# Performance work log

Hardware: AMD Instinct MI355X
Metric: run time of the kernel (lower is better)

The kernel has to match this reference:

```python
import jax, jax.numpy as jnp
import numpy as np

DIM, HEADS, RANK = 768, 12, 64
HEAD_DIM = DIM // HEADS

def _xavier(key, shape):
    fan_in, fan_out = shape[1], shape[0]
    std = (2.0 / (fan_in + fan_out)) ** 0.5
    return std * jax.random.normal(key, shape, dtype=jnp.float32)

def setup_inputs() -> dict:
    key = jax.random.key(0)
    ks = jax.random.split(key, 12)
    B, N = 8, 1024
    x = jax.random.normal(ks[0], (B, N, DIM), dtype=jnp.float32)
    params = {}
    for i, nm in enumerate(['Q', 'K', 'V']):
        params[f'W_{nm}0'] = _xavier(ks[1 + 3 * i], (DIM, RANK))
        params[f'W_{nm}1'] = _xavier(ks[2 + 3 * i], (HEADS, RANK))
        params[f'W_{nm}2'] = _xavier(ks[3 + 3 * i], (HEAD_DIM, RANK))
    proj_w = _xavier(ks[10], (DIM, DIM))
    proj_b = jnp.zeros((DIM,), dtype=jnp.float32)
    return dict(x=x, W_Q0=params['W_Q0'], W_Q1=params['W_Q1'], W_Q2=params['W_Q2'],
                W_K0=params['W_K0'], W_K1=params['W_K1'], W_K2=params['W_K2'],
                W_V0=params['W_V0'], W_V1=params['W_V1'], W_V2=params['W_V2'],
                proj_w=proj_w, proj_b=proj_b)

def _cp_proj(xh, W2, W1, W0, B, N, H, hd):
    # xh: [B,N,H,hd]; contract head_dim with W2 and heads with W1 -> [B,N,R], then expand to dim via W0
    t = jnp.einsum('blnd,dr,nr->blr', xh, W2, W1)
    out = jnp.einsum('blr,mr->blm', t, W0)          # [B,N,dim]
    return out.reshape(B, N, H, hd).transpose(0, 2, 1, 3)  # [B,H,N,hd]

def reference(x, W_Q0, W_Q1, W_Q2, W_K0, W_K1, W_K2, W_V0, W_V1, W_V2, proj_w, proj_b):
    B, N, C = x.shape
    H = W_Q1.shape[0]
    hd = C // H
    scale = hd ** -0.5
    xh = x.reshape(B, N, H, hd)
    q = _cp_proj(xh, W_Q2, W_Q1, W_Q0, B, N, H, hd)
    k = _cp_proj(xh, W_K2, W_K1, W_K0, B, N, H, hd)
    v = _cp_proj(xh, W_V2, W_V1, W_V0, B, N, H, hd)
    attn = jax.nn.softmax(jnp.einsum('bhqd,bhkd->bhqk', q, k) * scale, axis=-1)
    out = jnp.einsum('bhqk,bhkd->bhqd', attn, v).transpose(0, 2, 1, 3).reshape(B, N, C)
    return out @ proj_w.T + proj_b
```

## Files before the change

### kernel.cpp

```cpp
#include <hip/hip_runtime.h>

typedef unsigned short u16;
typedef __attribute__((ext_vector_type(8))) short bf16x8;
typedef __attribute__((ext_vector_type(4))) float f32x4;
typedef __attribute__((ext_vector_type(4))) unsigned short u16x4;
typedef __attribute__((ext_vector_type(8))) unsigned short u16x8;

#define AS1 __attribute__((address_space(1)))
#define AS3 __attribute__((address_space(3)))

__device__ __forceinline__ float b2f(u16 s) {
    return __uint_as_float(((unsigned)s) << 16);
}
__device__ __forceinline__ u16 f2b(float f) {
    unsigned u = __float_as_uint(f);
    unsigned r = 0x7fffu + ((u >> 16) & 1u);
    return (u16)((u + r) >> 16);
}

__device__ __forceinline__ unsigned packtrunc(float p0, float p1) {
#if __has_builtin(__builtin_amdgcn_perm)
    return __builtin_amdgcn_perm(__float_as_uint(p1), __float_as_uint(p0), 0x07060302u);
#else
    return (__float_as_uint(p0) >> 16) | (__float_as_uint(p1) & 0xffff0000u);
#endif
}

__device__ __forceinline__ void g2l16(const u16* g, u16* l) {
    __builtin_amdgcn_global_load_lds((const AS1 void*)g, (AS3 void*)l, 16, 0, 0);
}

#if __has_builtin(__builtin_amdgcn_exp2f)
#define EXP2(x) __builtin_amdgcn_exp2f(x)
#else
#define EXP2(x) exp2f(x)
#endif

__global__ __launch_bounds__(256) void build_prep(
    const float* __restrict__ Wq0, const float* __restrict__ Wq1, const float* __restrict__ Wq2,
    const float* __restrict__ Wk0, const float* __restrict__ Wk1, const float* __restrict__ Wk2,
    const float* __restrict__ Wv0, const float* __restrict__ Wv1, const float* __restrict__ Wv2,
    const float* __restrict__ PW,
    u16* __restrict__ G, u16* __restrict__ W0b, u16* __restrict__ Dcat)
{
    const int bx = blockIdx.x;
    const int t = threadIdx.x;
    if (bx < 1152) {
        const int idx = bx * 256 + t;
        if (idx < 147456) {
            const int row = idx / 768, c = idx - row * 768;
            const int which = row >> 6, r = row & 63;
            const int h = c >> 6, d = c & 63;
            const float* W1 = (which == 0) ? Wq1 : (which == 1) ? Wk1 : Wv1;
            const float* W2 = (which == 0) ? Wq2 : (which == 1) ? Wk2 : Wv2;
            G[idx] = f2b(W1[h * 64 + r] * W2[d * 64 + r]);
        } else {
            const int j = idx - 147456;
            const int row = j >> 6, r = j & 63;
            const int which = row / 768, mm = row - which * 768;
            const float* W0 = (which == 0) ? Wq0 : (which == 1) ? Wk0 : Wv0;
            const float scale = (which == 0) ? 0.125f * 1.4426950408889634f : 1.0f;
            W0b[j] = f2b(W0[mm * 64 + r] * scale);
        }
    } else {
        __shared__ float w0s[64 * 65];
        __shared__ float pws[32 * 65];
        const int hb = bx - 1152;
        const int h = hb / 24, mBase = (hb - h * 24) * 32;
        for (int i = t; i < 4096; i += 256) {
            const int d = i >> 6, r = i & 63;
            w0s[d * 65 + r] = Wv0[(h * 64 + d) * 64 + r];
        }
        for (int i = t; i < 2048; i += 256) {
            const int mi = i >> 6, d = i & 63;
            pws[mi * 65 + d] = PW[(size_t)(mBase + mi) * 768 + h * 64 + d];
        }
        __syncthreads();
        const int r = t & 63, mi0 = t >> 6;
        float w0c[64];
#pragma unroll
        for (int d = 0; d < 64; ++d) w0c[d] = w0s[d * 65 + r];
        for (int mi = mi0; mi < 32; mi += 4) {
            float acc = 0.f;
#pragma unroll
            for (int d = 0; d < 64; ++d) acc += pws[mi * 65 + d] * w0c[d];
            Dcat[(size_t)(mBase + mi) * 768 + h * 64 + r] = f2b(acc);
        }
    }
}

__global__ __launch_bounds__(256, 2) void gemm_t(
    const float* __restrict__ X, const u16* __restrict__ G,
    u16* __restrict__ T, u16* __restrict__ tvt)
{
    __shared__ u16 As[64 * 32];
    __shared__ u16 Bs[64 * 32];

    const int tid = threadIdx.x;
    const int lane = tid & 63, wv = tid >> 6;
    const int l15 = lane & 15, quad = lane >> 4;
    const int rowBase = blockIdx.y * 64;
    const int colBase = blockIdx.x * 64;

    const int srow = tid >> 2;
    const int scol = (tid & 3) * 8;
    const float* aS = X + (size_t)(rowBase + srow) * 768 + scol;
    const u16*  bS  = G + (size_t)(colBase + srow) * 768 + scol;

    float4 a0 = *(const float4*)(aS);
    float4 a1 = *(const float4*)(aS + 4);
    int4   b0 = *(const int4*)(bS);

    const f32x4 zero4 = {0.f, 0.f, 0.f, 0.f};
    f32x4 acc[4];
#pragma unroll
    for (int tn = 0; tn < 4; ++tn) acc[tn] = zero4;

    for (int kk = 0; kk < 768; kk += 32) {
        __syncthreads();
        u16x8 ap;
        ap[0] = f2b(a0.x); ap[1] = f2b(a0.y); ap[2] = f2b(a0.z); ap[3] = f2b(a0.w);
        ap[4] = f2b(a1.x); ap[5] = f2b(a1.y); ap[6] = f2b(a1.z); ap[7] = f2b(a1.w);
        *(u16x8*)&As[srow * 32 + scol] = ap;
        *(int4*)&Bs[srow * 32 + scol]  = b0;
        __syncthreads();

        if (kk < 736) {
            a0 = *(const float4*)(aS + kk + 32);
            a1 = *(const float4*)(aS + kk + 36);
            b0 = *(const int4*)(bS + kk + 32);
        }

        const bf16x8 af = *(const bf16x8*)(As + (wv * 16 + l15) * 32 + quad * 8);
#pragma unroll
        for (int tn = 0; tn < 4; ++tn) {
            const bf16x8 bf = *(const bf16x8*)(Bs + (tn * 16 + l15) * 32 + quad * 8);
            acc[tn] = __builtin_amdgcn_mfma_f32_16x16x32_bf16(af, bf, acc[tn], 0, 0, 0);
        }
    }

    if (colBase < 128) {
#pragma unroll
        for (int tn = 0; tn < 4; ++tn) {
            const int col = colBase + tn * 16 + l15;
#pragma unroll
            for (int r = 0; r < 4; ++r) {
                const int grow = rowBase + wv * 16 + quad * 4 + r;
                T[(size_t)grow * 128 + col] = f2b(acc[tn][r]);
            }
        }
    } else {
#pragma unroll
        for (int tn = 0; tn < 4; ++tn) {
            const int rr = tn * 16 + l15;
            const int grow = rowBase + wv * 16 + quad * 4;
            u16x4 pk;
            pk.x = f2b(acc[tn][0]); pk.y = f2b(acc[tn][1]);
            pk.z = f2b(acc[tn][2]); pk.w = f2b(acc[tn][3]);
            *(u16x4*)(tvt + (size_t)rr * 8192 + grow) = pk;
        }
    }
}

__global__ __launch_bounds__(256, 2) void gemm_expand(
    const u16* __restrict__ T, const u16* __restrict__ W0b, u16* __restrict__ qkp)
{
    __shared__ u16 As[128 * 32];
    __shared__ u16 Bs[128 * 32];

    const int tid  = threadIdx.x;
    const int lane = tid & 63, wv = tid >> 6;
    const int l15  = lane & 15, quad = lane >> 4;
    const int rowBase = blockIdx.y * 128;
    const int colBase = blockIdx.x * 128;
    const int which = blockIdx.x / 6;

    const int srow = wv * 32 + (lane >> 2);
    const int scol = (lane & 3) * 8;
    const u16* aSrc = T   + (size_t)(rowBase + srow) * 128 + which * 64 + scol;
    const u16* bSrc = W0b + (size_t)(colBase + srow) * 64 + scol;
    u16* aDst = As + wv * 1024;
    u16* bDst = Bs + wv * 1024;

    const f32x4 zero4 = {0.f, 0.f, 0.f, 0.f};
    f32x4 acc[4][4];
#pragma unroll
    for (int tm = 0; tm < 4; ++tm)
#pragma unroll
        for (int tn = 0; tn < 4; ++tn) acc[tm][tn] = zero4;

    const int wr = (wv >> 1) * 64, wc = (wv & 1) * 64;

    for (int kk = 0; kk < 64; kk += 32) {
        __syncthreads();
        g2l16(aSrc + kk,            aDst);
        g2l16(aSrc + kk + 16 * 128, aDst + 512);
        g2l16(bSrc + kk,            bDst);
        g2l16(bSrc + kk + 16 * 64,  bDst + 512);
        __syncthreads();

        bf16x8 af[4], bfm[4];
#pragma unroll
        for (int t = 0; t < 4; ++t) {
            af[t]  = *(const bf16x8*)(As + (wr + t * 16 + l15) * 32 + quad * 8);
            bfm[t] = *(const bf16x8*)(Bs + (wc + t * 16 + l15) * 32 + quad * 8);
        }
#pragma unroll
        for (int tm = 0; tm < 4; ++tm)
#pragma unroll
            for (int tn = 0; tn < 4; ++tn)
                acc[tm][tn] = __builtin_amdgcn_mfma_f32_16x16x32_bf16(
                    af[tm], bfm[tn], acc[tm][tn], 0, 0, 0);
    }

    const int mmBase = colBase - which * 768 + wc;
    u16* outp = qkp + (size_t)which * 6291456;
#pragma unroll
    for (int tm = 0; tm < 4; ++tm) {
        const int grow = rowBase + wr + tm * 16 + quad * 4;
        const int b = grow >> 10, l = grow & 1023;
#pragma unroll
        for (int tn = 0; tn < 4; ++tn) {
            const int mmv = mmBase + tn * 16 + l15;
            const int h = mmv >> 6, d = mmv & 63;
            const size_t base = (((size_t)(b * 12 + h) * 1024 + l) << 6) + d;
#pragma unroll
            for (int r = 0; r < 4; ++r)
                outp[base + (size_t)r * 64] = f2b(acc[tm][tn][r]);
        }
    }
}

__global__ __launch_bounds__(256, 3) void flash_attn6(
    const u16* __restrict__ qk, const u16* __restrict__ tvt, u16* __restrict__ Z)
{
    const int qt = blockIdx.x;
    const int bh = blockIdx.y;
    const int b = bh / 12, h = bh - b * 12;
    const u16* qp = qk + (size_t)bh * 65536 + qt * 8192;
    const u16* kp = qk + 6291456 + (size_t)bh * 65536;
    const u16* vp = tvt + b * 1024;

    __shared__ u16 Ks[64][72];
    __shared__ u16 Vs[64][72];

    const int t = threadIdx.x;
    const int lane = t & 63, wv = t >> 6;
    const int l15 = lane & 15, quad = lane >> 4;

    bf16x8 qf[2][2];
#pragma unroll
    for (int qg = 0; qg < 2; ++qg) {
        qf[qg][0] = *(const bf16x8*)(qp + (wv * 32 + qg * 16 + l15) * 64 + quad * 8);
        qf[qg][1] = *(const bf16x8*)(qp + (wv * 32 + qg * 16 + l15) * 64 + 32 + quad * 8);
    }

    const int srow = t >> 2;
    const int scol = (t & 3) * 16;
    const int p5 = srow & 31;
    const int lrow = (srow & 32) | ((p5 & 4) << 2) | ((p5 & 16) >> 1)
                   | ((p5 & 8) >> 1) | (p5 & 3);

    bf16x8 vone = {};
    if (l15 == 0) {
#pragma unroll
        for (int j = 0; j < 8; ++j) vone[j] = (short)0x3F80;
    }

    int4 kr0 = *(const int4*)(kp + srow * 64 + scol);
    int4 kr1 = *(const int4*)(kp + srow * 64 + scol + 8);
    int4 vr0 = *(const int4*)(vp + (size_t)srow * 8192 + scol);
    int4 vr1 = *(const int4*)(vp + (size_t)srow * 8192 + scol + 8);

    const f32x4 zero4 = {0.f, 0.f, 0.f, 0.f};
    f32x4 o_acc[2][4];
    f32x4 Lacc[2] = {zero4, zero4};
#pragma unroll
    for (int qg = 0; qg < 2; ++qg)
#pragma unroll
        for (int tn = 0; tn < 4; ++tn) o_acc[qg][tn] = zero4;

    for (int kt = 0; kt < 16; ++kt) {
        __syncthreads();
        *(int4*)&Ks[lrow][scol]     = kr0;
        *(int4*)&Ks[lrow][scol + 8] = kr1;
        *(int4*)&Vs[srow][scol]     = vr0;
        *(int4*)&Vs[srow][scol + 8] = vr1;
        __syncthreads();

        if (kt < 15) {
            kr0 = *(const int4*)(kp + (kt + 1) * 4096 + srow * 64 + scol);
            kr1 = *(const int4*)(kp + (kt + 1) * 4096 + srow * 64 + scol + 8);
            vr0 = *(const int4*)(vp + (size_t)srow * 8192 + (kt + 1) * 64 + scol);
            vr1 = *(const int4*)(vp + (size_t)srow * 8192 + (kt + 1) * 64 + scol + 8);
        }

        f32x4 Sacc[2][4];
#pragma unroll
        for (int qg = 0; qg < 2; ++qg)
#pragma unroll
            for (int tk = 0; tk < 4; ++tk) Sacc[qg][tk] = zero4;
#pragma unroll
        for (int ks = 0; ks < 2; ++ks) {
#pragma unroll
            for (int tk = 0; tk < 4; ++tk) {
                const bf16x8 kf = *(const bf16x8*)&Ks[tk * 16 + l15][ks * 32 + quad * 8];
                Sacc[0][tk] = __builtin_amdgcn_mfma_f32_16x16x32_bf16(kf, qf[0][ks], Sacc[0][tk], 0, 0, 0);
                Sacc[1][tk] = __builtin_amdgcn_mfma_f32_16x16x32_bf16(kf, qf[1][ks], Sacc[1][tk], 0, 0, 0);
            }
        }

        union { bf16x8 v; unsigned u[4]; } pf[2][2];
#pragma unroll
        for (int qg = 0; qg < 2; ++qg)
#pragma unroll
            for (int tk = 0; tk < 4; ++tk) {
                const float p0 = EXP2(Sacc[qg][tk][0]);
                const float p1 = EXP2(Sacc[qg][tk][1]);
                const float p2 = EXP2(Sacc[qg][tk][2]);
                const float p3 = EXP2(Sacc[qg][tk][3]);
                const int g = tk >> 1, hf = (tk & 1) * 2;
                pf[qg][g].u[hf + 0] = packtrunc(p0, p1);
                pf[qg][g].u[hf + 1] = packtrunc(p2, p3);
            }

#pragma unroll
        for (int g = 0; g < 2; ++g) {
#pragma unroll
            for (int tn = 0; tn < 4; ++tn) {
                const bf16x8 vf = *(const bf16x8*)&Vs[tn * 16 + l15][g * 32 + quad * 8];
                o_acc[0][tn] = __builtin_amdgcn_mfma_f32_16x16x32_bf16(pf[0][g].v, vf, o_acc[0][tn], 0, 0, 0);
                o_acc[1][tn] = __builtin_amdgcn_mfma_f32_16x16x32_bf16(pf[1][g].v, vf, o_acc[1][tn], 0, 0, 0);
            }
            Lacc[0] = __builtin_amdgcn_mfma_f32_16x16x32_bf16(pf[0][g].v, vone, Lacc[0], 0, 0, 0);
            Lacc[1] = __builtin_amdgcn_mfma_f32_16x16x32_bf16(pf[1][g].v, vone, Lacc[1], 0, 0, 0);
        }
    }

#pragma unroll
    for (int qg = 0; qg < 2; ++qg) {
#pragma unroll
        for (int r = 0; r < 4; ++r) {
            const float Lv = __shfl(Lacc[qg][r], quad << 4, 64);
            const float inv = 1.0f / Lv;
            const int token = qt * 128 + wv * 32 + qg * 16 + quad * 4 + r;
#pragma unroll
            for (int tn = 0; tn < 4; ++tn) {
                const int col = h * 64 + tn * 16 + l15;
                Z[(size_t)(b * 1024 + token) * 768 + col] = f2b(o_acc[qg][tn][r] * inv);
            }
        }
    }
}

__global__ __launch_bounds__(256, 3) void gemm_out(
    const u16* __restrict__ A, const u16* __restrict__ Bt,
    float* __restrict__ C, const float* __restrict__ bias)
{
    __shared__ u16 As[128 * 32];
    __shared__ u16 Bs[64 * 32];

    const int tid  = threadIdx.x;
    const int lane = tid & 63, wv = tid >> 6;
    const int l15  = lane & 15, quad = lane >> 4;
    const int rowBase = blockIdx.y * 128;
    const int colBase = blockIdx.x * 64;

    const int srowA = wv * 32 + (lane >> 2);
    const int srowB = wv * 16 + (lane >> 2);
    const int scol  = (lane & 3) * 8;
    const u16* aSrc = A  + (size_t)(rowBase + srowA) * 768 + scol;
    const u16* bSrc = Bt + (size_t)(colBase + srowB) * 768 + scol;
    u16* aDst = As + wv * 1024;
    u16* bDst = Bs + wv * 512;

    const f32x4 zero4 = {0.f, 0.f, 0.f, 0.f};
    f32x4 acc[2][4];
#pragma unroll
    for (int tm = 0; tm < 2; ++tm)
#pragma unroll
        for (int tn = 0; tn < 4; ++tn) acc[tm][tn] = zero4;

    for (int kk = 0; kk < 768; kk += 32) {
        __syncthreads();
        g2l16(aSrc + kk,            aDst);
        g2l16(aSrc + kk + 16 * 768, aDst + 512);
        g2l16(bSrc + kk,            bDst);
        __syncthreads();

        bf16x8 af[2], bfm[4];
#pragma unroll
        for (int t = 0; t < 2; ++t)
            af[t]  = *(const bf16x8*)(As + (wv * 32 + t * 16 + l15) * 32 + quad * 8);
#pragma unroll
        for (int t = 0; t < 4; ++t)
            bfm[t] = *(const bf16x8*)(Bs + (t * 16 + l15) * 32 + quad * 8);
#pragma unroll
        for (int tm = 0; tm < 2; ++tm)
#pragma unroll
            for (int tn = 0; tn < 4; ++tn)
                acc[tm][tn] = __builtin_amdgcn_mfma_f32_16x16x32_bf16(
                    af[tm], bfm[tn], acc[tm][tn], 0, 0, 0);
    }

#pragma unroll
    for (int tm = 0; tm < 2; ++tm) {
        const int grow = rowBase + wv * 32 + tm * 16 + quad * 4;
#pragma unroll
        for (int tn = 0; tn < 4; ++tn) {
            const int gcol = colBase + tn * 16 + l15;
            const float bv = bias[gcol];
#pragma unroll
            for (int r = 0; r < 4; ++r)
                C[(size_t)(grow + r) * 768 + gcol] = acc[tm][tn][r] + bv;
        }
    }
}

extern "C" void kernel_launch(void* const* d_in, const int* in_sizes, int n_in,
                              void* d_out, int out_size, void* d_ws, size_t ws_size,
                              hipStream_t stream)
{
    const float* x      = (const float*)d_in[0];
    const float* Wq0    = (const float*)d_in[1];
    const float* Wq1    = (const float*)d_in[2];
    const float* Wq2    = (const float*)d_in[3];
    const float* Wk0    = (const float*)d_in[4];
    const float* Wk1    = (const float*)d_in[5];
    const float* Wk2    = (const float*)d_in[6];
    const float* Wv0    = (const float*)d_in[7];
    const float* Wv1    = (const float*)d_in[8];
    const float* Wv2    = (const float*)d_in[9];
    const float* proj_w = (const float*)d_in[10];
    const float* proj_b = (const float*)d_in[11];
    float* outp = (float*)d_out;

    char* ws = (char*)d_ws;
    u16* T    = (u16*)ws;
    u16* tvt  = (u16*)(ws + 2097152);
    u16* G    = (u16*)(ws + 3145728);
    u16* W0b  = (u16*)(ws + 3440640);
    u16* Dcat = (u16*)(ws + 3735552);
    u16* Zcat = (u16*)(ws + 4915200);
    u16* qk   = (u16*)(ws + 17498112);

    build_prep<<<1440, 256, 0, stream>>>(Wq0, Wq1, Wq2, Wk0, Wk1, Wk2, Wv0, Wv1, Wv2,
                                         proj_w, G, W0b, Dcat);
    gemm_t<<<dim3(3, 128), 256, 0, stream>>>(x, G, T, tvt);
    gemm_expand<<<dim3(12, 64), 256, 0, stream>>>(T, W0b, qk);
    flash_attn6<<<dim3(8, 96), 256, 0, stream>>>(qk, tvt, Zcat);
    gemm_out<<<dim3(12, 64), 256, 0, stream>>>(Zcat, Dcat, outp, proj_b);
}
```

Before: 180.1 us.

## Fold Q expansion into per-head rank-space key matrix, skip Q materialization

Precomputes per-head M_h = Wq0_h^T Wk0_h (scaled) in rank space, so queries stay as the rank-64 T vectors and only K' = T_k M_h^T is expanded. This halves the expand GEMM grid and removes writing and reading the full Q tensor. Attention now reads Q rows straight from T with a 128-element stride. The grid order of the attention kernel is also swapped so blocks sharing a batch run together. Rounding changes because the combined weight is stored in bf16.

```diff
diff --git a/kernel.cpp b/kernel.cpp
--- a/kernel.cpp
+++ b/kernel.cpp
@@ -41,31 +41,40 @@
     const float* __restrict__ Wk0, const float* __restrict__ Wk1, const float* __restrict__ Wk2,
     const float* __restrict__ Wv0, const float* __restrict__ Wv1, const float* __restrict__ Wv2,
     const float* __restrict__ PW,
-    u16* __restrict__ G, u16* __restrict__ W0b, u16* __restrict__ Dcat)
+    u16* __restrict__ G, u16* __restrict__ Mqkb, u16* __restrict__ Dcat)
 {
     const int bx = blockIdx.x;
     const int t = threadIdx.x;
-    if (bx < 1152) {
+    if (bx < 576) {
         const int idx = bx * 256 + t;
-        if (idx < 147456) {
-            const int row = idx / 768, c = idx - row * 768;
-            const int which = row >> 6, r = row & 63;
-            const int h = c >> 6, d = c & 63;
-            const float* W1 = (which == 0) ? Wq1 : (which == 1) ? Wk1 : Wv1;
-            const float* W2 = (which == 0) ? Wq2 : (which == 1) ? Wk2 : Wv2;
-            G[idx] = f2b(W1[h * 64 + r] * W2[d * 64 + r]);
-        } else {
-            const int j = idx - 147456;
-            const int row = j >> 6, r = j & 63;
-            const int which = row / 768, mm = row - which * 768;
-            const float* W0 = (which == 0) ? Wq0 : (which == 1) ? Wk0 : Wv0;
-            const float scale = (which == 0) ? 0.125f * 1.4426950408889634f : 1.0f;
-            W0b[j] = f2b(W0[mm * 64 + r] * scale);
+        const int row = idx / 768, c = idx - row * 768;
+        const int which = row >> 6, r = row & 63;
+        const int h = c >> 6, d = c & 63;
+        const float* W1 = (which == 0) ? Wq1 : (which == 1) ? Wk1 : Wv1;
+        const float* W2 = (which == 0) ? Wq2 : (which == 1) ? Wk2 : Wv2;
+        G[idx] = f2b(W1[h * 64 + r] * W2[d * 64 + r]);
+    } else if (bx < 588) {
+        __shared__ float wq[64 * 65];
+        __shared__ float wk[64 * 65];
+        const int h = bx - 576;
+        const float qs = 0.125f * 1.4426950408889634f;
+        for (int i = t; i < 4096; i += 256) {
+            const int dd = i >> 6, r = i & 63;
+            wq[dd * 65 + r] = Wq0[(h * 64 + dd) * 64 + r] * qs;
+            wk[dd * 65 + r] = Wk0[(h * 64 + dd) * 64 + r];
+        }
+        __syncthreads();
+        for (int j = t; j < 4096; j += 256) {
+            const int r1 = j >> 6, r2 = j & 63;
+            float acc = 0.f;
+#pragma unroll
+            for (int dd = 0; dd < 64; ++dd) acc += wq[dd * 65 + r1] * wk[dd * 65 + r2];
+            Mqkb[(size_t)(h * 64 + r1) * 64 + r2] = f2b(acc);
         }
     } else {
         __shared__ float w0s[64 * 65];
         __shared__ float pws[32 * 65];
-        const int hb = bx - 1152;
+        const int hb = bx - 588;
         const int h = hb / 24, mBase = (hb - h * 24) * 32;
         for (int i = t; i < 4096; i += 256) {
             const int d = i >> 6, r = i & 63;
@@ -163,7 +172,7 @@
 }
 
 __global__ __launch_bounds__(256, 2) void gemm_expand(
-    const u16* __restrict__ T, const u16* __restrict__ W0b, u16* __restrict__ qkp)
+    const u16* __restrict__ T, const u16* __restrict__ Mqkb, u16* __restrict__ kp)
 {
     __shared__ u16 As[128 * 32];
     __shared__ u16 Bs[128 * 32];
@@ -173,12 +182,11 @@
     const int l15  = lane & 15, quad = lane >> 4;
     const int rowBase = blockIdx.y * 128;
     const int colBase = blockIdx.x * 128;
-    const int which = blockIdx.x / 6;
 
     const int srow = wv * 32 + (lane >> 2);
     const int scol = (lane & 3) * 8;
-    const u16* aSrc = T   + (size_t)(rowBase + srow) * 128 + which * 64 + scol;
-    const u16* bSrc = W0b + (size_t)(colBase + srow) * 64 + scol;
+    const u16* aSrc = T    + (size_t)(rowBase + srow) * 128 + 64 + scol;
+    const u16* bSrc = Mqkb + (size_t)(colBase + srow) * 64 + scol;
     u16* aDst = As + wv * 1024;
     u16* bDst = Bs + wv * 1024;
 
@@ -213,8 +221,7 @@
                     af[tm], bfm[tn], acc[tm][tn], 0, 0, 0);
     }
 
-    const int mmBase = colBase - which * 768 + wc;
-    u16* outp = qkp + (size_t)which * 6291456;
+    const int mmBase = colBase + wc;
 #pragma unroll
     for (int tm = 0; tm < 4; ++tm) {
         const int grow = rowBase + wr + tm * 16 + quad * 4;
@@ -222,23 +229,24 @@
 #pragma unroll
         for (int tn = 0; tn < 4; ++tn) {
             const int mmv = mmBase + tn * 16 + l15;
-            const int h = mmv >> 6, d = mmv & 63;
-            const size_t base = (((size_t)(b * 12 + h) * 1024 + l) << 6) + d;
+            const int h = mmv >> 6, r1 = mmv & 63;
+            const size_t base = (((size_t)(b * 12 + h) * 1024 + l) << 6) + r1;
 #pragma unroll
             for (int r = 0; r < 4; ++r)
-                outp[base + (size_t)r * 64] = f2b(acc[tm][tn][r]);
-        }
-    }
-}
-
-__global__ __launch_bounds__(256, 3) void flash_attn6(
-    const u16* __restrict__ qk, const u16* __restrict__ tvt, u16* __restrict__ Z)
-{
-    const int qt = blockIdx.x;
-    const int bh = blockIdx.y;
+                kp[base + (size_t)r * 64] = f2b(acc[tm][tn][r]);
+        }
+    }
+}
+
+__global__ __launch_bounds__(256, 3) void flash_attn7(
+    const u16* __restrict__ T, const u16* __restrict__ kprime,
+    const u16* __restrict__ tvt, u16* __restrict__ Z)
+{
+    const int bh = blockIdx.x;
+    const int qt = blockIdx.y;
     const int b = bh / 12, h = bh - b * 12;
-    const u16* qp = qk + (size_t)bh * 65536 + qt * 8192;
-    const u16* kp = qk + 6291456 + (size_t)bh * 65536;
+    const u16* qp = T + ((size_t)b * 1024 + qt * 128) * 128;
+    const u16* kp = kprime + (size_t)bh * 65536;
     const u16* vp = tvt + b * 1024;
 
     __shared__ u16 Ks[64][72];
@@ -251,8 +259,9 @@
     bf16x8 qf[2][2];
 #pragma unroll
     for (int qg = 0; qg < 2; ++qg) {
-        qf[qg][0] = *(const bf16x8*)(qp + (wv * 32 + qg * 16 + l15) * 64 + quad * 8);
-        qf[qg][1] = *(const bf16x8*)(qp + (wv * 32 + qg * 16 + l15) * 64 + 32 + quad * 8);
+        const u16* qrow = qp + (size_t)(wv * 32 + qg * 16 + l15) * 128;
+        qf[qg][0] = *(const bf16x8*)(qrow + quad * 8);
+        qf[qg][1] = *(const bf16x8*)(qrow + 32 + quad * 8);
     }
 
     const int srow = t >> 2;
@@ -439,15 +448,15 @@
     u16* T    = (u16*)ws;
     u16* tvt  = (u16*)(ws + 2097152);
     u16* G    = (u16*)(ws + 3145728);
-    u16* W0b  = (u16*)(ws + 3440640);
-    u16* Dcat = (u16*)(ws + 3735552);
-    u16* Zcat = (u16*)(ws + 4915200);
-    u16* qk   = (u16*)(ws + 17498112);
-
-    build_prep<<<1440, 256, 0, stream>>>(Wq0, Wq1, Wq2, Wk0, Wk1, Wk2, Wv0, Wv1, Wv2,
-                                         proj_w, G, W0b, Dcat);
+    u16* Mqkb = (u16*)(ws + 3440640);
+    u16* Dcat = (u16*)(ws + 3538944);
+    u16* Zcat = (u16*)(ws + 4718592);
+    u16* kp   = (u16*)(ws + 17301504);
+
+    build_prep<<<876, 256, 0, stream>>>(Wq0, Wq1, Wq2, Wk0, Wk1, Wk2, Wv0, Wv1, Wv2,
+                                        proj_w, G, Mqkb, Dcat);
     gemm_t<<<dim3(3, 128), 256, 0, stream>>>(x, G, T, tvt);
-    gemm_expand<<<dim3(12, 64), 256, 0, stream>>>(T, W0b, qk);
-    flash_attn6<<<dim3(8, 96), 256, 0, stream>>>(qk, tvt, Zcat);
+    gemm_expand<<<dim3(6, 64), 256, 0, stream>>>(T, Mqkb, kp);
+    flash_attn7<<<dim3(96, 8), 256, 0, stream>>>(T, kp, tvt, Zcat);
     gemm_out<<<dim3(12, 64), 256, 0, stream>>>(Zcat, Dcat, outp, proj_b);
 }
```

New measurement: 182.0 us. Within noise of the previous version (+1.1%).
